# Performance work log

Hardware: AMD Instinct MI355X
Metric: run time of the kernel (lower is better)

The kernel has to match this reference:

```python
import jax, jax.numpy as jnp
import numpy as np

D_MODEL, D_INNER, D_CONV, D_STATE, DT_RANK = 1024, 2048, 4, 16, 64
B_SZ, L = 2, 2048


def setup_inputs() -> dict:
    key = jax.random.key(0)
    ks = jax.random.split(key, 8)
    s = 0.02
    x = jax.random.normal(ks[0], (B_SZ, L, D_MODEL), jnp.float32)
    in_proj_w = jax.random.normal(ks[1], (D_MODEL, 2 * D_INNER), jnp.float32) * s
    conv_w = jax.random.normal(ks[2], (D_INNER, 1, D_CONV), jnp.float32) * 0.1
    conv_b = jax.random.normal(ks[3], (D_INNER,), jnp.float32) * 0.1
    x_proj_w = jax.random.normal(ks[4], (D_INNER, DT_RANK + 2 * D_STATE), jnp.float32) * s
    dt_proj_w = jax.random.normal(ks[5], (DT_RANK, D_INNER), jnp.float32) * s
    dt_proj_b = jax.random.normal(ks[6], (D_INNER,), jnp.float32) * 0.1
    A_log = jnp.log(jnp.broadcast_to(jnp.arange(1, D_STATE + 1, dtype=jnp.float32), (D_INNER, D_STATE)))
    D = jnp.ones((D_INNER,), jnp.float32)
    out_proj_w = jax.random.normal(ks[7], (D_INNER, D_MODEL), jnp.float32) * s
    return dict(x=x, in_proj_w=in_proj_w, conv_w=conv_w, conv_b=conv_b,
                x_proj_w=x_proj_w, dt_proj_w=dt_proj_w, dt_proj_b=dt_proj_b,
                A_log=A_log, D=D, out_proj_w=out_proj_w)


def _selective_scan(u, delta, A, B, C, D):
    # u, delta: (b,l,d); A: (d,n); B,C: (b,l,n); D: (d,)
    b, l, d = u.shape
    n = A.shape[1]
    deltaA = jnp.exp(jnp.einsum('bld,dn->bldn', delta, A))          # (b,l,d,n)
    deltaB_u = jnp.einsum('bld,bln,bld->bldn', delta, B, u)          # (b,l,d,n)

    def step(xc, inputs):
        dA_t, dBu_t, C_t = inputs                                     # (b,d,n),(b,d,n),(b,n)
        xc = dA_t * xc + dBu_t
        y_t = jnp.einsum('bdn,bn->bd', xc, C_t)
        return xc, y_t

    x0 = jnp.zeros((b, d, n), u.dtype)
    _, ys = jax.lax.scan(step, x0, (deltaA.transpose(1, 0, 2, 3),
                                    deltaB_u.transpose(1, 0, 2, 3),
                                    C.transpose(1, 0, 2)))
    return ys.transpose(1, 0, 2) + u * D


def reference(x, in_proj_w, conv_w, conv_b, x_proj_w, dt_proj_w, dt_proj_b, A_log, D, out_proj_w):
    b, l, _ = x.shape
    xr = x @ in_proj_w                                                # (b,l,2*d_inner)
    xi, res = jnp.split(xr, 2, axis=-1)
    # causal depthwise conv1d (torch pads both sides by d_conv-1 then slices [:l])
    xc = jax.lax.conv_general_dilated(
        xi.transpose(0, 2, 1), conv_w, window_strides=(1,),
        padding=[(D_CONV - 1, 0)], feature_group_count=D_INNER,
        dimension_numbers=('NCH', 'OIH', 'NCH')) + conv_b[None, :, None]
    xc = jax.nn.silu(xc.transpose(0, 2, 1))                           # (b,l,d_inner)
    # SSM
    A = -jnp.exp(A_log)
    x_dbl = xc @ x_proj_w                                             # (b,l,dt_rank+2n)
    dt, Bm, Cm = jnp.split(x_dbl, [DT_RANK, DT_RANK + D_STATE], axis=-1)
    delta = jax.nn.softplus(dt @ dt_proj_w + dt_proj_b)               # (b,l,d_inner)
    y = _selective_scan(xc, delta, A, Bm, Cm, D)
    y = y * jax.nn.silu(res)
    return y @ out_proj_w
```

## Files before the change

kernel.cpp:

```cpp
#include <hip/hip_runtime.h>
#include <hip/hip_bf16.h>

#define D_MODEL 1024
#define D_INNER 2048
#define D_CONV  4
#define D_STATE 16
#define DT_RANK 64
#define B_SZ    2
#define SEQ_L   2048
#define BLROWS  (B_SZ * SEQ_L)

#define NCHUNK  32
#define CHUNK   (SEQ_L / NCHUNK)

#define XP_N    96
#define XP_SPLIT 8
#define XP_KCH  (D_INNER / XP_SPLIT)

typedef __hip_bfloat16 bf16;
typedef __attribute__((ext_vector_type(8))) short bshort8;
typedef __attribute__((ext_vector_type(4))) float f32x4;

__device__ __forceinline__ float b2f(bf16 v) { return __bfloat162float(v); }
__device__ __forceinline__ bf16  f2b(float v) { return __float2bfloat16(v); }
__device__ __forceinline__ short f2s(float v) {
    bf16 h = __float2bfloat16(v);
    return *reinterpret_cast<short*>(&h);
}
__device__ __forceinline__ float s2f(short s) {
    unsigned u = ((unsigned)(unsigned short)s) << 16;
    float f; __builtin_memcpy(&f, &u, 4); return f;
}
__device__ __forceinline__ float siluf(float x) { return x / (1.f + __expf(-x)); }
__device__ __forceinline__ float softplusf(float x) {
    return fmaxf(x, 0.f) + log1pf(__expf(-fabsf(x)));
}
__device__ __forceinline__ float exp_neg(float a) { return __expf(fminf(a, 0.f)); }

__device__ __forceinline__ void gl2lds16(const bf16* g, bf16* l) {
    __builtin_amdgcn_global_load_lds((const __attribute__((address_space(1))) void*)g,
                                     (__attribute__((address_space(3))) void*)l,
                                     16, 0, 0);
}

#define N_X    (B_SZ * SEQ_L * D_MODEL)
#define N_IPW  (D_MODEL * 2 * D_INNER)
#define N_CW   (D_INNER * D_CONV)
#define N_CB   (D_INNER)
#define N_XPW  (D_INNER * (DT_RANK + 2*D_STATE))
#define N_DTW  (DT_RANK * D_INNER)
#define N_DTB  (D_INNER)
#define N_AL   (D_INNER * D_STATE)
#define N_D    (D_INNER)
#define N_OPW  (D_INNER * D_MODEL)

#define S0 ((long)N_X)
#define S1 (S0 + N_IPW)
#define S2 (S1 + N_CW)
#define S3 (S2 + N_CB)
#define S4 (S3 + N_XPW)
#define S5 (S4 + N_DTW)
#define S6 (S5 + N_DTB)
#define S7 (S6 + N_AL)
#define S8 (S7 + N_D)
#define S9 (S8 + N_OPW)

#define PP_CVT   1024
#define PP_T0    4096
#define PP_T1    192
#define PP_T2    128
#define PP_T3    2048
#define PP_TOTAL (PP_CVT + PP_T0 + PP_T1 + PP_T2 + PP_T3)

__global__ __launch_bounds__(256)
void preprocess_kernel(int* __restrict__ flag,
                       const void* p0, const void* p1, const void* p2,
                       const void* p3, const void* p4, const void* p5,
                       const void* p6, const void* p7, const void* p8,
                       const void* p9,
                       bf16* __restrict__ canon,
                       bf16* __restrict__ d_ipw, bf16* __restrict__ d_xpw,
                       bf16* __restrict__ d_dtw, bf16* __restrict__ d_opw)
{
    __shared__ float tile[32][33];
    const float* al = (const float*)p7;
    const bool f32 = (fabsf(al[1] - 0.6931472f) < 0.05f) && (fabsf(al[0]) < 1e-3f);

    if (blockIdx.x == 0 && threadIdx.x == 0) {
        int fast = f32 ? 1 : 0;
        if (f32) {
            const int rows[3] = {0, 513, 1023};
            for (int i = 0; i < 3 && fast; ++i)
                for (int n = 0; n < D_STATE; ++n)
                    if (fabsf(al[rows[i] * D_STATE + n] - logf((float)(n + 1))) > 2e-3f)
                        { fast = 0; break; }
        }
        flag[0] = f32 ? 1 : 0;
        flag[1] = fast;
    }

    int bid = blockIdx.x;
    if (bid < PP_CVT) {
        const long total4 = S9 / 4;
        for (long i4 = (long)bid * 256 + threadIdx.x; i4 < total4;
             i4 += (long)PP_CVT * 256) {
            long idx = i4 * 4;
            const void* src; long lo; bool keep = true;
            if      (idx < S0) { src = p0; lo = idx; }
            else if (idx < S1) { src = p1; lo = idx - S0; keep = false; }
            else if (idx < S2) { src = p2; lo = idx - S1; }
            else if (idx < S3) { src = p3; lo = idx - S2; }
            else if (idx < S4) { src = p4; lo = idx - S3; keep = false; }
            else if (idx < S5) { src = p5; lo = idx - S4; keep = false; }
            else if (idx < S6) { src = p6; lo = idx - S5; }
            else if (idx < S7) { src = p7; lo = idx - S6; }
            else if (idx < S8) { src = p8; lo = idx - S7; }
            else               { src = p9; lo = idx - S8; keep = false; }
            if (!keep) continue;
            ushort4 o;
            if (f32) {
                float4 v = ((const float4*)src)[lo >> 2];
                o.x = (unsigned short)f2s(v.x); o.y = (unsigned short)f2s(v.y);
                o.z = (unsigned short)f2s(v.z); o.w = (unsigned short)f2s(v.w);
            } else {
                o = ((const ushort4*)src)[lo >> 2];
            }
            ((ushort4*)canon)[idx >> 2] = o;
        }
        return;
    }

    bid -= PP_CVT;
    const void* src; bf16* dst; int R, C, txt;
    if (bid < PP_T0)      { src = p1; dst = d_ipw; R = D_MODEL; C = 2 * D_INNER; txt = 128; }
    else if ((bid -= PP_T0) < PP_T1) { src = p4; dst = d_xpw; R = D_INNER; C = XP_N;    txt = 3;  }
    else if ((bid -= PP_T1) < PP_T2) { src = p5; dst = d_dtw; R = DT_RANK; C = D_INNER; txt = 64; }
    else                  { bid -= PP_T2; src = p9; dst = d_opw; R = D_INNER; C = D_MODEL; txt = 32; }

    const int r0 = (bid / txt) * 32, c0 = (bid % txt) * 32;
    const int tx = threadIdx.x & 31, ty = threadIdx.x >> 5;

    #pragma unroll
    for (int p = 0; p < 4; ++p) {
        int r = r0 + ty + p * 8, c = c0 + tx;
        float v = 0.f;
        if (r < R && c < C)
            v = f32 ? ((const float*)src)[(size_t)r * C + c]
                    : b2f(((const bf16*)src)[(size_t)r * C + c]);
        tile[ty + p * 8][tx] = v;
    }
    __syncthreads();
    #pragma unroll
    for (int p = 0; p < 4; ++p) {
        int c = c0 + ty + p * 8, r = r0 + tx;
        if (c < C && r < R)
            dst[(size_t)c * R + r] = f2b(tile[tx][ty + p * 8]);
    }
}

__global__ __launch_bounds__(256)
void gemm_mfma_bt_kernel(const bf16* __restrict__ A, int lda,
                         const bf16* __restrict__ BT, int ldb,
                         void* __restrict__ C, int ldc,
                         int M, int N, int K,
                         const bf16* __restrict__ bias, int mode,
                         const int* __restrict__ flag,
                         void* __restrict__ C2)
{
    __shared__ __align__(16) bf16 As[2][128 * 32];
    __shared__ __align__(16) bf16 Bs[2][128 * 32];

    const int tid  = threadIdx.x;
    const int wave = tid >> 6;
    const int lane = tid & 63;
    const int t    = lane & 15;
    const int q    = lane >> 4;
    const int wm   = wave & 1;
    const int wn   = wave >> 1;

    const int row0 = blockIdx.y * 128;
    const int col0 = blockIdx.x * 128;

    const int s_row = (lane >> 2);
    const int s_col = (lane & 3) * 8;
    const bool stageA = (wave < 2);
    const int  sw     = stageA ? wave : (wave - 2);
    const bf16* g_base = stageA ? A : BT;
    const int   g_ld   = stageA ? lda : ldb;
    const int   g_row0 = (stageA ? row0 : col0) + sw * 64 + s_row;

    f32x4 acc[4][4] = {};
    const int outf32 = (mode == 2) ? flag[0] : 0;

    for (int k0 = 0; k0 < K; k0 += 64) {
        #pragma unroll
        for (int h = 0; h < 2; ++h) {
            bf16* l_base = (stageA ? As[h] : Bs[h]) + (size_t)sw * 2048;
            #pragma unroll
            for (int c = 0; c < 4; ++c) {
                const bf16* g = g_base + (size_t)(g_row0 + c * 16) * g_ld
                                + k0 + h * 32 + s_col;
                gl2lds16(g, l_base + c * 512);
            }
        }
        __syncthreads();

        #pragma unroll
        for (int h = 0; h < 2; ++h) {
            bshort8 aF[4], bF[4];
            #pragma unroll
            for (int i = 0; i < 4; ++i)
                aF[i] = *(const bshort8*)&As[h][((wm * 64 + i * 16 + t) << 5) + (q << 3)];
            #pragma unroll
            for (int j = 0; j < 4; ++j)
                bF[j] = *(const bshort8*)&Bs[h][((wn * 64 + j * 16 + t) << 5) + (q << 3)];

            #pragma unroll
            for (int i = 0; i < 4; ++i)
                #pragma unroll
                for (int j = 0; j < 4; ++j)
                    acc[i][j] = __builtin_amdgcn_mfma_f32_16x16x32_bf16(
                                    aF[i], bF[j], acc[i][j], 0, 0, 0);
        }
        __syncthreads();
    }

    #pragma unroll
    for (int i = 0; i < 4; ++i) {
        #pragma unroll
        for (int j = 0; j < 4; ++j) {
            const int c_g = col0 + wn * 64 + j * 16 + t;
            const int r_b = row0 + wm * 64 + i * 16 + q * 4;
            #pragma unroll
            for (int r = 0; r < 4; ++r) {
                const int r_g = r_b + r;
                float v = acc[i][j][r];
                if (mode == 1) {
                    v += b2f(bias[c_g]);
                    ((bf16*)C)[(size_t)r_g * ldc + c_g] = f2b(softplusf(v));
                } else if (mode == 2) {
                    size_t o = (size_t)r_g * ldc + c_g;
                    if (outf32) ((float*)C)[o] = v;
                    else        ((bf16*)C)[o]  = f2b(v);
                } else if (mode == 3) {
                    if (c_g < D_INNER)
                        ((bf16*)C )[(size_t)r_g * D_INNER + c_g] = f2b(v);
                    else
                        ((bf16*)C2)[(size_t)r_g * D_INNER + (c_g - D_INNER)] = f2b(v);
                } else {
                    ((bf16*)C)[(size_t)r_g * ldc + c_g] = f2b(v);
                }
            }
        }
    }
}

__global__ __launch_bounds__(256)
void gemm_mfma_bt64_kernel(const bf16* __restrict__ A, int lda,
                           const bf16* __restrict__ BT, int ldb,
                           void* __restrict__ C, int ldc,
                           int M, int N, int K,
                           const bf16* __restrict__ bias, int mode,
                           const int* __restrict__ flag)
{
    __shared__ __align__(16) bf16 As[2][64 * 32];
    __shared__ __align__(16) bf16 Bs[2][128 * 32];

    const int tid  = threadIdx.x;
    const int wave = tid >> 6;
    const int lane = tid & 63;
    const int t    = lane & 15;
    const int q    = lane >> 4;
    const int wm   = wave & 1;
    const int wn   = wave >> 1;

    const int row0 = blockIdx.y * 64;
    const int col0 = blockIdx.x * 128;

    const int s_row = lane >> 2;
    const int s_col = (lane & 3) * 8;

    f32x4 acc[2][4] = {};
    const int outf32 = (mode == 2) ? flag[0] : 0;

    for (int k0 = 0; k0 < K; k0 += 64) {
        #pragma unroll
        for (int h = 0; h < 2; ++h) {
            if (wave < 2) {
                #pragma unroll
                for (int c = 0; c < 2; ++c) {
                    const bf16* g = A + (size_t)(row0 + wave * 32 + c * 16 + s_row) * lda
                                    + k0 + h * 32 + s_col;
                    gl2lds16(g, As[h] + (wave * 32 + c * 16) * 32);
                }
            } else {
                #pragma unroll
                for (int c = 0; c < 4; ++c) {
                    const bf16* g = BT + (size_t)(col0 + (wave - 2) * 64 + c * 16 + s_row) * ldb
                                    + k0 + h * 32 + s_col;
                    gl2lds16(g, Bs[h] + ((wave - 2) * 64 + c * 16) * 32);
                }
            }
        }
        __syncthreads();

        #pragma unroll
        for (int h = 0; h < 2; ++h) {
            bshort8 aF[2], bF[4];
            #pragma unroll
            for (int i = 0; i < 2; ++i)
                aF[i] = *(const bshort8*)&As[h][((wm * 32 + i * 16 + t) << 5) + (q << 3)];
            #pragma unroll
            for (int j = 0; j < 4; ++j)
                bF[j] = *(const bshort8*)&Bs[h][((wn * 64 + j * 16 + t) << 5) + (q << 3)];

            #pragma unroll
            for (int i = 0; i < 2; ++i)
                #pragma unroll
                for (int j = 0; j < 4; ++j)
                    acc[i][j] = __builtin_amdgcn_mfma_f32_16x16x32_bf16(
                                    aF[i], bF[j], acc[i][j], 0, 0, 0);
        }
        __syncthreads();
    }

    #pragma unroll
    for (int i = 0; i < 2; ++i) {
        #pragma unroll
        for (int j = 0; j < 4; ++j) {
            const int c_g = col0 + wn * 64 + j * 16 + t;
            const int r_b = row0 + wm * 32 + i * 16 + q * 4;
            #pragma unroll
            for (int r = 0; r < 4; ++r) {
                const int r_g = r_b + r;
                float v = acc[i][j][r];
                if (mode == 1) {
                    v += b2f(bias[c_g]);
                    ((bf16*)C)[(size_t)r_g * ldc + c_g] = f2b(softplusf(v));
                } else {
                    size_t o = (size_t)r_g * ldc + c_g;
                    if (outf32) ((float*)C)[o] = v;
                    else        ((bf16*)C)[o]  = f2b(v);
                }
            }
        }
    }
}

__global__ __launch_bounds__(256)
void xproj_splitk_kernel(const bf16* __restrict__ A,
                         const bf16* __restrict__ BT,
                         float* __restrict__ part)
{
    __shared__ __align__(16) bf16 As[2][128 * 32];
    __shared__ __align__(16) bf16 Bs[2][XP_N * 32];

    const int tid  = threadIdx.x;
    const int wave = tid >> 6;
    const int lane = tid & 63;
    const int t    = lane & 15;
    const int q    = lane >> 4;

    const int row0 = blockIdx.x * 128;
    const int s    = blockIdx.y;
    const int kbeg = s * XP_KCH;

    const int s_row = lane >> 2;
    const int s_col = (lane & 3) * 8;

    f32x4 acc[2][6] = {};

    for (int k0 = kbeg; k0 < kbeg + XP_KCH; k0 += 64) {
        #pragma unroll
        for (int h = 0; h < 2; ++h) {
            if (wave < 2) {
                #pragma unroll
                for (int c = 0; c < 4; ++c) {
                    const bf16* g = A + (size_t)(row0 + wave * 64 + c * 16 + s_row) * D_INNER
                                    + k0 + h * 32 + s_col;
                    gl2lds16(g, As[h] + (wave * 64 + c * 16) * 32);
                }
            } else {
                const int nb = (wave == 2) ? 4 : 2;
                for (int c = 0; c < nb; ++c) {
                    const bf16* g = BT + (size_t)((wave - 2) * 64 + c * 16 + s_row) * D_INNER
                                    + k0 + h * 32 + s_col;
                    gl2lds16(g, Bs[h] + ((wave - 2) * 64 + c * 16) * 32);
                }
            }
        }
        __syncthreads();

        #pragma unroll
        for (int h = 0; h < 2; ++h) {
            bshort8 aF[2], bF[6];
            #pragma unroll
            for (int i = 0; i < 2; ++i)
                aF[i] = *(const bshort8*)&As[h][((wave * 32 + i * 16 + t) << 5) + (q << 3)];
            #pragma unroll
            for (int j = 0; j < 6; ++j)
                bF[j] = *(const bshort8*)&Bs[h][((j * 16 + t) << 5) + (q << 3)];

            #pragma unroll
            for (int i = 0; i < 2; ++i)
                #pragma unroll
                for (int j = 0; j < 6; ++j)
                    acc[i][j] = __builtin_amdgcn_mfma_f32_16x16x32_bf16(
                                    aF[i], bF[j], acc[i][j], 0, 0, 0);
        }
        __syncthreads();
    }

    #pragma unroll
    for (int i = 0; i < 2; ++i) {
        #pragma unroll
        for (int j = 0; j < 6; ++j) {
            const int c_g = j * 16 + t;
            const int r_b = row0 + wave * 32 + i * 16 + q * 4;
            #pragma unroll
            for (int r = 0; r < 4; ++r)
                part[((size_t)s * BLROWS + (r_b + r)) * XP_N + c_g] = acc[i][j][r];
        }
    }
}

__global__ __launch_bounds__(256)
void xproj_reduce_kernel(const float* __restrict__ part, bf16* __restrict__ xdbl)
{
    int idx = blockIdx.x * 256 + threadIdx.x;
    if (idx >= BLROWS * XP_N) return;
    float v = 0.f;
    #pragma unroll
    for (int s = 0; s < XP_SPLIT; ++s)
        v += part[(size_t)s * BLROWS * XP_N + idx];
    xdbl[idx] = f2b(v);
}

__global__ __launch_bounds__(256)
void conv_silu_kernel(const bf16* __restrict__ xi,
                      const bf16* __restrict__ cw,
                      const bf16* __restrict__ cb,
                      bf16* __restrict__ xc)
{
    int idx = blockIdx.x * 256 + threadIdx.x;
    const int total = BLROWS * (D_INNER / 8);
    if (idx >= total) return;
    const int d8 = idx % (D_INNER / 8);
    const int bl = idx / (D_INNER / 8);
    const int l  = bl % SEQ_L;
    const int b  = bl / SEQ_L;
    const int d0 = d8 * 8;

    bshort8 cv[4];
    #pragma unroll
    for (int v = 0; v < 4; ++v)
        cv[v] = ((const bshort8*)(cw + (size_t)d0 * 4))[v];

    bshort8 bv = *(const bshort8*)(cb + d0);
    float acc[8];
    #pragma unroll
    for (int e = 0; e < 8; ++e) acc[e] = s2f(bv[e]);

    #pragma unroll
    for (int k = 0; k < D_CONV; ++k) {
        int tt = l + k - (D_CONV - 1);
        if (tt >= 0) {
            bshort8 xv = *(const bshort8*)(xi + ((size_t)b * SEQ_L + tt) * D_INNER + d0);
            #pragma unroll
            for (int e = 0; e < 8; ++e) {
                const int f = e * 4 + k;
                acc[e] += s2f(xv[e]) * s2f(cv[f >> 3][f & 7]);
            }
        }
    }
    bshort8 ov;
    #pragma unroll
    for (int e = 0; e < 8; ++e) {
        float a = acc[e];
        ov[e] = f2s(a * (1.f / (1.f + __expf(-a))));
    }
    *(bshort8*)(xc + (size_t)bl * D_INNER + d0) = ov;
}

__global__ __launch_bounds__(256)
void scan_p1_kernel(const bf16* delta, const bf16* xc, const bf16* xdbl,
                    const bf16* A_log,
                    float* state, float* sumdelta,
                    const int* flags)
{
    __shared__ float Bsh[CHUNK][D_STATE];
    const int tid = threadIdx.x;
    const int d = blockIdx.x * 256 + tid;
    const int c = blockIdx.y;
    const int b = blockIdx.z;
    const int row0 = b * SEQ_L + c * CHUNK;
    const int fastA = flags[1];

    for (int e = tid; e < CHUNK * D_STATE; e += 256) {
        int t = e / D_STATE, n = e % D_STATE;
        Bsh[t][n] = b2f(xdbl[(size_t)(row0 + t) * 96 + DT_RANK + n]);
    }
    __syncthreads();

    float A[D_STATE];
    if (!fastA) {
        #pragma unroll
        for (int n = 0; n < D_STATE; ++n) A[n] = -__expf(b2f(A_log[d * D_STATE + n]));
    }

    float x[D_STATE] = {};
    float S = 0.f;
    if (fastA) {
        for (int t = 0; t < CHUNK; ++t) {
            size_t r = row0 + t;
            float dt_v = b2f(delta[r * D_INNER + d]);
            float u    = b2f(xc[r * D_INNER + d]);
            float bu = dt_v * u;
            S += dt_v;
            float e1 = __expf(-fmaxf(dt_v, 0.f));
            float p = e1;
            #pragma unroll
            for (int n = 0; n < D_STATE; ++n) {
                x[n] = p * x[n] + Bsh[t][n] * bu;
                p *= e1;
            }
        }
    } else {
        for (int t = 0; t < CHUNK; ++t) {
            size_t r = row0 + t;
            float dt_v = b2f(delta[r * D_INNER + d]);
            float u    = b2f(xc[r * D_INNER + d]);
            float bu = dt_v * u;
            S += dt_v;
            #pragma unroll
            for (int n = 0; n < D_STATE; ++n)
                x[n] = exp_neg(dt_v * A[n]) * x[n] + Bsh[t][n] * bu;
        }
    }
    size_t o = ((size_t)(b * NCHUNK + c) * D_INNER + d) * D_STATE;
    #pragma unroll
    for (int n = 0; n < D_STATE; ++n) state[o + n] = x[n];
    sumdelta[(size_t)(b * NCHUNK + c) * D_INNER + d] = S;
}

__global__ __launch_bounds__(256)
void scan_p2_kernel(const bf16* A_log, float* state, const float* sumdelta)
{
    int idx = blockIdx.x * 256 + threadIdx.x;
    int n  = idx & (D_STATE - 1);
    int dn = idx >> 4;
    int d  = dn & (D_INNER - 1);
    int b  = dn >> 11;

    float A_n = -__expf(b2f(A_log[d * D_STATE + n]));
    float carry = 0.f;
    #pragma unroll 4
    for (int c = 0; c < NCHUNK; ++c) {
        size_t o = ((size_t)(b * NCHUNK + c) * D_INNER + d) * D_STATE + n;
        float local = state[o];
        float S = sumdelta[(size_t)(b * NCHUNK + c) * D_INNER + d];
        state[o] = carry;
        carry = exp_neg(A_n * S) * carry + local;
    }
}

__global__ __launch_bounds__(256)
void scan_p3_kernel(const bf16* delta, bf16* xc, const bf16* xdbl,
                    const bf16* res,
                    const bf16* A_log, const bf16* Dvec,
                    const float* state,
                    const int* flags)
{
    __shared__ float Bsh[CHUNK][D_STATE];
    __shared__ float Csh[CHUNK][D_STATE];
    const int tid = threadIdx.x;
    const int d = blockIdx.x * 256 + tid;
    const int c = blockIdx.y;
    const int b = blockIdx.z;
    const int row0 = b * SEQ_L + c * CHUNK;
    const int fastA = flags[1];

    for (int e = tid; e < CHUNK * 2 * D_STATE; e += 256) {
        int t = e / (2 * D_STATE), j = e % (2 * D_STATE);
        float v = b2f(xdbl[(size_t)(row0 + t) * 96 + DT_RANK + j]);
        if (j < D_STATE) Bsh[t][j] = v;
        else             Csh[t][j - D_STATE] = v;
    }
    __syncthreads();

    float A[D_STATE];
    if (!fastA) {
        #pragma unroll
        for (int n = 0; n < D_STATE; ++n) A[n] = -__expf(b2f(A_log[d * D_STATE + n]));
    }
    const float Dd = b2f(Dvec[d]);

    float x[D_STATE];
    size_t o = ((size_t)(b * NCHUNK + c) * D_INNER + d) * D_STATE;
    #pragma unroll
    for (int n = 0; n < D_STATE; ++n) x[n] = state[o + n];

    if (fastA) {
        for (int t = 0; t < CHUNK; ++t) {
            size_t r = row0 + t;
            float dt_v = b2f(delta[r * D_INNER + d]);
            float u    = b2f(xc[r * D_INNER + d]);
            float resv = b2f(res[r * D_INNER + d]);
            float bu = dt_v * u;
            float e1 = __expf(-fmaxf(dt_v, 0.f));
            float p = e1;
            float dot = 0.f;
            #pragma unroll
            for (int n = 0; n < D_STATE; ++n) {
                x[n] = p * x[n] + Bsh[t][n] * bu;
                p *= e1;
                dot += x[n] * Csh[t][n];
            }
            float y = (dot + u * Dd) * siluf(resv);
            xc[r * D_INNER + d] = f2b(y);
        }
    } else {
        for (int t = 0; t < CHUNK; ++t) {
            size_t r = row0 + t;
            float dt_v = b2f(delta[r * D_INNER + d]);
            float u    = b2f(xc[r * D_INNER + d]);
            float resv = b2f(res[r * D_INNER + d]);
            float bu = dt_v * u;
            float dot = 0.f;
            #pragma unroll
            for (int n = 0; n < D_STATE; ++n) {
                x[n] = exp_neg(dt_v * A[n]) * x[n] + Bsh[t][n] * bu;
                dot += x[n] * Csh[t][n];
            }
            float y = (dot + u * Dd) * siluf(resv);
            xc[r * D_INNER + d] = f2b(y);
        }
    }
}

extern "C" void kernel_launch(void* const* d_in, const int* in_sizes, int n_in,
                              void* d_out, int out_size, void* d_ws, size_t ws_size,
                              hipStream_t stream)
{
    char* ws = (char*)d_ws;
    int*  flag  = (int*)ws;
    bf16* canon = (bf16*)(ws + 64);

    bf16* c_x    = canon;
    bf16* c_ipwT = canon + S0;
    bf16* c_cw   = canon + S1;
    bf16* c_cb   = canon + S2;
    bf16* c_xpwT = canon + S3;
    bf16* c_dtwT = canon + S4;
    bf16* c_dtb  = canon + S5;
    bf16* c_al   = canon + S6;
    bf16* c_d    = canon + S7;
    bf16* c_opwT = canon + S8;

    char* p = ws + 64 + (size_t)S9 * sizeof(bf16);
    bf16* xi    = (bf16*)p;  p += (size_t)BLROWS * D_INNER * sizeof(bf16);
    bf16* xc    = (bf16*)p;  p += (size_t)BLROWS * D_INNER * sizeof(bf16);
    bf16* res   = (bf16*)p;  p += (size_t)BLROWS * D_INNER * sizeof(bf16);
    bf16* xdbl  = (bf16*)p;  p += (size_t)BLROWS * 96 * sizeof(bf16);
    bf16* delta = (bf16*)p;  p += (size_t)BLROWS * D_INNER * sizeof(bf16);
    float* sumdelta = (float*)p; p += (size_t)B_SZ * NCHUNK * D_INNER * 4;
    float* xp_part = (float*)xi;
    float* state   = (float*)xi;
    bf16* ybuf = xc;

    dim3 blk(256);

    preprocess_kernel<<<dim3(PP_TOTAL), blk, 0, stream>>>(
        flag, d_in[0], d_in[1], d_in[2], d_in[3], d_in[4],
        d_in[5], d_in[6], d_in[7], d_in[8], d_in[9],
        canon, c_ipwT, c_xpwT, c_dtwT, c_opwT);

    {
        dim3 g((2 * D_INNER) / 128, BLROWS / 128);
        gemm_mfma_bt_kernel<<<g, blk, 0, stream>>>(c_x, D_MODEL, c_ipwT, D_MODEL,
                                                   xi, D_INNER,
                                                   BLROWS, 2 * D_INNER, D_MODEL,
                                                   nullptr, 3, flag, res);
    }
    {
        int total = BLROWS * (D_INNER / 8);
        conv_silu_kernel<<<dim3((total + 255) / 256), blk, 0, stream>>>(xi, c_cw, c_cb, xc);
    }
    {
        dim3 g1(BLROWS / 128, XP_SPLIT);
        xproj_splitk_kernel<<<g1, blk, 0, stream>>>(xc, c_xpwT, xp_part);
        dim3 g2((BLROWS * XP_N) / 256);
        xproj_reduce_kernel<<<g2, blk, 0, stream>>>(xp_part, xdbl);
    }
    {
        dim3 g(D_INNER / 128, BLROWS / 64);
        gemm_mfma_bt64_kernel<<<g, blk, 0, stream>>>(xdbl, 96, c_dtwT, DT_RANK,
                                                     delta, D_INNER,
                                                     BLROWS, D_INNER, DT_RANK,
                                                     c_dtb, 1, flag);
    }
    {
        dim3 g1(D_INNER / 256, NCHUNK, B_SZ);
        scan_p1_kernel<<<g1, blk, 0, stream>>>(delta, xc, xdbl, c_al, state, sumdelta, flag);
        dim3 g2((B_SZ * D_INNER * D_STATE) / 256);
        scan_p2_kernel<<<g2, blk, 0, stream>>>(c_al, state, sumdelta);
        scan_p3_kernel<<<g1, blk, 0, stream>>>(delta, xc, xdbl, res, c_al, c_d, state, flag);
    }
    {
        dim3 g(D_MODEL / 128, BLROWS / 64);
        gemm_mfma_bt64_kernel<<<g, blk, 0, stream>>>(ybuf, D_INNER, c_opwT, D_INNER,
                                                     d_out, D_MODEL,
                                                     BLROWS, D_MODEL, D_INNER,
                                                     nullptr, 2, flag);
    }
}
```

Before: 348.5 us.

## Replace in_proj GEMM with 256x256-tile pipelined MFMA kernel with swizzled LDS

Swaps the generic 128x128 in-projection GEMM for a dedicated kernel that uses 256x256 tiles, 512 threads and a BK of 64. Global-to-LDS copies are double-buffered and interleaved with MFMA work under explicit waitcnt and barrier control. The kernel also XOR-swizzles LDS to avoid bank conflicts, raises wave priority around the MFMAs, and remaps workgroup IDs for cache locality. This is meant to raise data reuse and overlap memory with compute on the largest GEMM, but the hand-written waitcnt counts add correctness risk, and with only 256 blocks occupancy may be low.

```diff
diff --git a/kernel.cpp b/kernel.cpp
--- a/kernel.cpp
+++ b/kernel.cpp
@@ -158,98 +158,125 @@
     }
 }
 
-__global__ __launch_bounds__(256)
-void gemm_mfma_bt_kernel(const bf16* __restrict__ A, int lda,
-                         const bf16* __restrict__ BT, int ldb,
-                         void* __restrict__ C, int ldc,
-                         int M, int N, int K,
-                         const bf16* __restrict__ bias, int mode,
-                         const int* __restrict__ flag,
-                         void* __restrict__ C2)
-{
-    __shared__ __align__(16) bf16 As[2][128 * 32];
-    __shared__ __align__(16) bf16 Bs[2][128 * 32];
+#define IP_NT (D_MODEL / 64)
+
+#define IP_STA(nb, k0n, s)                                                    \
+    { _Pragma("unroll") for (int c = 0; c < 2; ++c) {                         \
+        const int rr = aR + (s) * 64 + c * 8;                                 \
+        gl2lds16(A + (size_t)(row0 + rr + lr) * D_MODEL + (k0n) + slot * 8,   \
+                 &As[nb][rr * 64]); } }
+
+#define IP_STB(nb, k0n, s)                                                    \
+    { _Pragma("unroll") for (int c = 0; c < 2; ++c) {                         \
+        const int rr = bR + (s) * 16 + c * 8;                                 \
+        gl2lds16(BT + (size_t)(col0 + rr + lr) * D_MODEL + (k0n) + slot * 8,  \
+                 &Bs[nb][rr * 64]); } }
+
+#define IP_LDB(cb)                                                            \
+    { _Pragma("unroll") for (int j = 0; j < 4; ++j) {                         \
+        bF[j][0] = *(const bshort8*)&Bs[cb][(wn*64 + j*16 + t15)*64 + fc0];   \
+        bF[j][1] = *(const bshort8*)&Bs[cb][(wn*64 + j*16 + t15)*64 + fc1]; } }
+
+#define IP_LDA(cb, i0)                                                        \
+    { _Pragma("unroll") for (int ii = 0; ii < 2; ++ii) {                      \
+        aF[ii][0] = *(const bshort8*)&As[cb][(wm*128 + ((i0)+ii)*16 + t15)*64 + fc0]; \
+        aF[ii][1] = *(const bshort8*)&As[cb][(wm*128 + ((i0)+ii)*16 + t15)*64 + fc1]; } }
+
+#define IP_MMA(i0)                                                            \
+    __builtin_amdgcn_s_setprio(1);                                            \
+    { _Pragma("unroll") for (int ii = 0; ii < 2; ++ii)                        \
+      _Pragma("unroll") for (int j = 0; j < 4; ++j)                           \
+      _Pragma("unroll") for (int h = 0; h < 2; ++h)                           \
+        acc[(i0)+ii][j] = __builtin_amdgcn_mfma_f32_16x16x32_bf16(            \
+            aF[ii][h], bF[j][h], acc[(i0)+ii][j], 0, 0, 0); }                 \
+    __builtin_amdgcn_s_setprio(0);
+
+__global__ __launch_bounds__(512, 2)
+void gemm_inproj256_kernel(const bf16* __restrict__ A,
+                           const bf16* __restrict__ BT,
+                           bf16* __restrict__ C1,
+                           bf16* __restrict__ C2)
+{
+    __shared__ __align__(16) bf16 As[2][256 * 64];
+    __shared__ __align__(16) bf16 Bs[2][256 * 64];
 
     const int tid  = threadIdx.x;
     const int wave = tid >> 6;
     const int lane = tid & 63;
-    const int t    = lane & 15;
+    const int t15  = lane & 15;
     const int q    = lane >> 4;
-    const int wm   = wave & 1;
-    const int wn   = wave >> 1;
-
-    const int row0 = blockIdx.y * 128;
-    const int col0 = blockIdx.x * 128;
-
-    const int s_row = (lane >> 2);
-    const int s_col = (lane & 3) * 8;
-    const bool stageA = (wave < 2);
-    const int  sw     = stageA ? wave : (wave - 2);
-    const bf16* g_base = stageA ? A : BT;
-    const int   g_ld   = stageA ? lda : ldb;
-    const int   g_row0 = (stageA ? row0 : col0) + sw * 64 + s_row;
-
-    f32x4 acc[4][4] = {};
-    const int outf32 = (mode == 2) ? flag[0] : 0;
-
-    for (int k0 = 0; k0 < K; k0 += 64) {
-        #pragma unroll
-        for (int h = 0; h < 2; ++h) {
-            bf16* l_base = (stageA ? As[h] : Bs[h]) + (size_t)sw * 2048;
-            #pragma unroll
-            for (int c = 0; c < 4; ++c) {
-                const bf16* g = g_base + (size_t)(g_row0 + c * 16) * g_ld
-                                + k0 + h * 32 + s_col;
-                gl2lds16(g, l_base + c * 512);
-            }
-        }
-        __syncthreads();
-
-        #pragma unroll
-        for (int h = 0; h < 2; ++h) {
-            bshort8 aF[4], bF[4];
-            #pragma unroll
-            for (int i = 0; i < 4; ++i)
-                aF[i] = *(const bshort8*)&As[h][((wm * 64 + i * 16 + t) << 5) + (q << 3)];
-            #pragma unroll
-            for (int j = 0; j < 4; ++j)
-                bF[j] = *(const bshort8*)&Bs[h][((wn * 64 + j * 16 + t) << 5) + (q << 3)];
-
-            #pragma unroll
-            for (int i = 0; i < 4; ++i)
-                #pragma unroll
-                for (int j = 0; j < 4; ++j)
-                    acc[i][j] = __builtin_amdgcn_mfma_f32_16x16x32_bf16(
-                                    aF[i], bF[j], acc[i][j], 0, 0, 0);
-        }
-        __syncthreads();
-    }
-
-    #pragma unroll
-    for (int i = 0; i < 4; ++i) {
+    const int wm   = wave >> 2;
+    const int wn   = wave & 3;
+
+    int wg = blockIdx.x;
+    wg = (wg & 7) * 32 + (wg >> 3);
+    const int row0 = (wg >> 4) * 256;
+    const int col0 = (wg & 15) * 256;
+
+    const int lr   = lane >> 3;
+    const int slot = (lane & 7) ^ lr;
+    const int aR   = wm * 128 + wn * 16;
+    const int bR   = wn * 64  + wm * 32;
+    const int x7   = t15 & 7;
+    const int fc0  = ((0 + q) ^ x7) * 8;
+    const int fc1  = ((4 + q) ^ x7) * 8;
+
+    f32x4 acc[8][4] = {};
+    bshort8 bF[4][2], aF[2][2];
+
+    IP_STB(0, 0, 0); IP_STB(0, 0, 1); IP_STA(0, 0, 0); IP_STA(0, 0, 1);
+
+    for (int t = 0; t < IP_NT - 1; ++t) {
+        const int cb = t & 1, nb = cb ^ 1;
+        const int k0n = (t + 1) * 64;
+        asm volatile("s_waitcnt vmcnt(2)" ::: "memory");
+        __builtin_amdgcn_s_barrier();
+        __builtin_amdgcn_sched_barrier(0);
+        IP_LDB(cb);
+        IP_LDA(cb, 0);
+        IP_STB(nb, k0n, 0);
+        IP_MMA(0);
+        IP_LDA(cb, 2);
+        IP_STB(nb, k0n, 1);
+        IP_MMA(2);
+        asm volatile("s_waitcnt vmcnt(4)" ::: "memory");
+        __builtin_amdgcn_s_barrier();
+        __builtin_amdgcn_sched_barrier(0);
+        IP_LDA(cb, 4);
+        IP_STA(nb, k0n, 0);
+        IP_MMA(4);
+        IP_LDA(cb, 6);
+        IP_STA(nb, k0n, 1);
+        IP_MMA(6);
+        asm volatile("s_waitcnt lgkmcnt(0)" ::: "memory");
+    }
+    {
+        const int cb = (IP_NT - 1) & 1;
+        asm volatile("s_waitcnt vmcnt(2)" ::: "memory");
+        __builtin_amdgcn_s_barrier();
+        __builtin_amdgcn_sched_barrier(0);
+        IP_LDB(cb);
+        IP_LDA(cb, 0); IP_MMA(0);
+        IP_LDA(cb, 2); IP_MMA(2);
+        asm volatile("s_waitcnt vmcnt(0)" ::: "memory");
+        __builtin_amdgcn_s_barrier();
+        __builtin_amdgcn_sched_barrier(0);
+        IP_LDA(cb, 4); IP_MMA(4);
+        IP_LDA(cb, 6); IP_MMA(6);
+    }
+    #pragma unroll
+    for (int i = 0; i < 8; ++i) {
         #pragma unroll
         for (int j = 0; j < 4; ++j) {
-            const int c_g = col0 + wn * 64 + j * 16 + t;
-            const int r_b = row0 + wm * 64 + i * 16 + q * 4;
+            const int c_g = col0 + wn * 64 + j * 16 + t15;
+            const int r_b = row0 + wm * 128 + i * 16 + q * 4;
             #pragma unroll
             for (int r = 0; r < 4; ++r) {
-                const int r_g = r_b + r;
-                float v = acc[i][j][r];
-                if (mode == 1) {
-                    v += b2f(bias[c_g]);
-                    ((bf16*)C)[(size_t)r_g * ldc + c_g] = f2b(softplusf(v));
-                } else if (mode == 2) {
-                    size_t o = (size_t)r_g * ldc + c_g;
-                    if (outf32) ((float*)C)[o] = v;
-                    else        ((bf16*)C)[o]  = f2b(v);
-                } else if (mode == 3) {
-                    if (c_g < D_INNER)
-                        ((bf16*)C )[(size_t)r_g * D_INNER + c_g] = f2b(v);
-                    else
-                        ((bf16*)C2)[(size_t)r_g * D_INNER + (c_g - D_INNER)] = f2b(v);
-                } else {
-                    ((bf16*)C)[(size_t)r_g * ldc + c_g] = f2b(v);
-                }
+                const float v = acc[i][j][r];
+                if (c_g < D_INNER)
+                    C1[(size_t)(r_b + r) * D_INNER + c_g] = f2b(v);
+                else
+                    C2[(size_t)(r_b + r) * D_INNER + (c_g - D_INNER)] = f2b(v);
             }
         }
     }
@@ -675,13 +702,8 @@
         d_in[5], d_in[6], d_in[7], d_in[8], d_in[9],
         canon, c_ipwT, c_xpwT, c_dtwT, c_opwT);
 
-    {
-        dim3 g((2 * D_INNER) / 128, BLROWS / 128);
-        gemm_mfma_bt_kernel<<<g, blk, 0, stream>>>(c_x, D_MODEL, c_ipwT, D_MODEL,
-                                                   xi, D_INNER,
-                                                   BLROWS, 2 * D_INNER, D_MODEL,
-                                                   nullptr, 3, flag, res);
-    }
+    gemm_inproj256_kernel<<<dim3(256), dim3(512), 0, stream>>>(c_x, c_ipwT, xi, res);
+
     {
         int total = BLROWS * (D_INNER / 8);
         conv_silu_kernel<<<dim3((total + 255) / 256), blk, 0, stream>>>(xi, c_cw, c_cb, xc);
```

After: 309.4 us. 11.2% less time.
